# Performance work log

Measured on AMD Instinct MI355X. Metric: run time of the kernel, lower is better.

Reference implementation:

```python
import jax, jax.numpy as jnp
import numpy as np

NMOD, NVEC, R, M, B = 4, 100000, 64, 512, 16384


def setup_inputs() -> dict:
    key = jax.random.key(0)
    ks = jax.random.split(key, 9)
    indices = jax.random.randint(ks[0], (B, NMOD), 0, NVEC, dtype=jnp.int32)
    # logit(U(0,1)) init for v_hat tables
    def logit_init(k):
        u = jax.random.uniform(k, (NVEC, R), dtype=jnp.float32, minval=1e-4, maxval=1.0 - 1e-4)
        return jnp.log(u) - jnp.log1p(-u)
    v0, v1, v2, v3 = (logit_init(ks[i]) for i in range(1, 5))
    S = jax.random.normal(ks[5], (M, NMOD * R), dtype=jnp.float32) / (2 * np.pi)
    b = jax.random.uniform(ks[6], (1, M), dtype=jnp.float32, minval=0.0, maxval=2 * np.pi)
    w_mu = jax.random.uniform(ks[7], (2 * M, 1), dtype=jnp.float32)
    return {"indices": indices, "v0": v0, "v1": v1, "v2": v2, "v3": v3,
            "S": S, "b": b, "w_mu": w_mu}


def _stick_break_gather(v_hat, idx):
    # Stick-breaking weights are computed row-wise (cumsum over axis=1),
    # so gathering rows first is mathematically identical to building the
    # full table and gathering (and far cheaper).
    vh = v_hat[idx]                       # [B, R]
    log_v = jax.nn.log_sigmoid(vh)
    log_vm = jax.nn.log_sigmoid(-vh)
    excl_cumsum = jnp.cumsum(log_vm, axis=1) - log_vm  # exclusive cumsum
    return jnp.exp(log_v + excl_cumsum)   # [B, R]


def reference(indices, v0, v1, v2, v3, S, b, w_mu):
    emb = jnp.concatenate([
        _stick_break_gather(v0, indices[:, 0]),
        _stick_break_gather(v1, indices[:, 1]),
        _stick_break_gather(v2, indices[:, 2]),
        _stick_break_gather(v3, indices[:, 3]),
    ], axis=1)                             # [B, 4R]
    phi_lin = emb @ S.T + b                # [B, M]
    phi = jnp.concatenate([jnp.cos(phi_lin), jnp.sin(phi_lin)], axis=1)  # [B, 2M]
    return jax.nn.sigmoid(phi @ w_mu)      # [B, 1]
```

## Files before the change

kernel.cpp:

```cpp
#include <hip/hip_runtime.h>
#include <math.h>

#define B_TOTAL 16384
#define RR 64
#define KK 256
#define MM 512
#define ROWS 32
#define NCH 8
#define NNI 4
#define MI 2
#define ASTR 264
#define INV2PI 0.15915494309189535f

typedef __attribute__((ext_vector_type(8))) _Float16 half8;
typedef __attribute__((ext_vector_type(4))) float floatx4;

template<int CTRL, int RMASK>
static __device__ inline float dpp_mov1(float src) {
    int s = __builtin_bit_cast(int, src);
    int o = __builtin_bit_cast(int, 1.0f);
    int r = __builtin_amdgcn_update_dpp(o, s, CTRL, RMASK, 0xF, false);
    return __builtin_bit_cast(float, r);
}
template<int CTRL>
static __device__ inline float dpp_swap(float src) {
    int s = __builtin_bit_cast(int, src);
    int r = __builtin_amdgcn_update_dpp(s, s, CTRL, 0xF, 0xF, false);
    return __builtin_bit_cast(float, r);
}
static __device__ inline float red16(float x) {
    x += dpp_swap<0xB1>(x);
    x += dpp_swap<0x4E>(x);
    x += dpp_swap<0x141>(x);
    x += dpp_swap<0x140>(x);
    return x;
}

__global__ __launch_bounds__(256)
void conv_S(const float* __restrict__ S, _Float16* __restrict__ Bh)
{
    const int F = blockIdx.x * 256 + threadIdx.x;
    const int o = F >> 9;
    const int c = F & 511;
    const float* src = &S[c * KK + o * 8];
    float v[8];
    *reinterpret_cast<float4*>(&v[0]) = *reinterpret_cast<const float4*>(src);
    *reinterpret_cast<float4*>(&v[4]) = *reinterpret_cast<const float4*>(src + 4);
    half8 hv;
    #pragma unroll
    for (int j = 0; j < 8; ++j)
        hv[j] = (_Float16)(v[j] * INV2PI);
    *reinterpret_cast<half8*>(&Bh[F * 8]) = hv;
}

__global__ __launch_bounds__(512, 4)
void nest2_mfma(const int* __restrict__ indices,
                const float* __restrict__ v0, const float* __restrict__ v1,
                const float* __restrict__ v2, const float* __restrict__ v3,
                const _Float16* __restrict__ Bh,
                const float* __restrict__ bvec, const float* __restrict__ w_mu,
                float* __restrict__ out)
{
    __shared__ alignas(16) _Float16 Ah[ROWS * ASTR];
    __shared__ float red[8][ROWS];

    const int tid = threadIdx.x;
    const int rowBase = blockIdx.x * ROWS;
    const int wid  = __builtin_amdgcn_readfirstlane(tid >> 6);
    const int lane = tid & 63;
    const int l15  = lane & 15;
    const int lg   = lane >> 4;
    const int wcol0 = wid * 64;

    #define BOFF(ch, ni) ((((ch) * 4 + lg) * 512 + wcol0 + (ni) * 16 + l15) * 8)

    const int* ip = indices + rowBase * 4 + wid * 16;
    const float* vts[4] = {v0, v1, v2, v3};
    float vh[16];
    #pragma unroll
    for (int it = 0; it < 16; ++it) {
        const int mod = it & 3;
        vh[it] = vts[mod][ip[it] * RR + lane];
    }

    half8 b[NNI];
    #pragma unroll
    for (int ni = 0; ni < NNI; ++ni)
        b[ni] = *reinterpret_cast<const half8*>(&Bh[BOFF(0, ni)]);
    float bbv[NNI], wav[NNI];
    #pragma unroll
    for (int ni = 0; ni < NNI; ++ni) {
        const int c = wcol0 + ni * 16 + l15;
        const float w1 = w_mu[c];
        const float w2 = w_mu[MM + c];
        wav[ni] = sqrtf(w1 * w1 + w2 * w2);
        bbv[ni] = bvec[c] * INV2PI + atan2f(w1, w2) * INV2PI;
    }

    #pragma unroll
    for (int it = 0; it < 16; ++it) {
        const int p   = wid * 16 + it;
        const int row = p >> 2;
        const int mod = p & 3;
        const float t  = __expf(vh[it]);
        const float um = __builtin_amdgcn_rcpf(1.f + t);
        float pr = um;
        pr *= dpp_mov1<0x111, 0xF>(pr);
        pr *= dpp_mov1<0x112, 0xF>(pr);
        pr *= dpp_mov1<0x114, 0xF>(pr);
        pr *= dpp_mov1<0x118, 0xF>(pr);
        pr *= dpp_mov1<0x142, 0xA>(pr);
        pr *= dpp_mov1<0x143, 0xC>(pr);
        const float x = t * pr;
        Ah[row * ASTR + mod * RR + lane] = (_Float16)x;
    }
    __syncthreads();

    floatx4 acc[MI][NNI];
    #pragma unroll
    for (int mi = 0; mi < MI; ++mi)
        #pragma unroll
        for (int ni = 0; ni < NNI; ++ni)
            acc[mi][ni] = (floatx4){0.f, 0.f, 0.f, 0.f};

    #pragma unroll
    for (int ch = 0; ch < NCH; ++ch) {
        half8 ah[MI];
        #pragma unroll
        for (int mi = 0; mi < MI; ++mi)
            ah[mi] = *reinterpret_cast<const half8*>(
                &Ah[(mi * 16 + l15) * ASTR + ch * 32 + lg * 8]);
        half8 bn[NNI];
        if (ch + 1 < NCH) {
            #pragma unroll
            for (int ni = 0; ni < NNI; ++ni)
                bn[ni] = *reinterpret_cast<const half8*>(&Bh[BOFF(ch + 1, ni)]);
        }
        __builtin_amdgcn_s_setprio(1);
        #pragma unroll
        for (int ni = 0; ni < NNI; ++ni)
            #pragma unroll
            for (int mi = 0; mi < MI; ++mi)
                acc[mi][ni] = __builtin_amdgcn_mfma_f32_16x16x32_f16(ah[mi], b[ni], acc[mi][ni], 0, 0, 0);
        __builtin_amdgcn_s_setprio(0);
        if (ch + 1 < NCH) {
            #pragma unroll
            for (int ni = 0; ni < NNI; ++ni)
                b[ni] = bn[ni];
        }
    }

    float rp[MI][4];
    #pragma unroll
    for (int mi = 0; mi < MI; ++mi)
        #pragma unroll
        for (int r = 0; r < 4; ++r) rp[mi][r] = 0.f;

    #pragma unroll
    for (int ni = 0; ni < NNI; ++ni) {
        #pragma unroll
        for (int mi = 0; mi < MI; ++mi)
            #pragma unroll
            for (int r = 0; r < 4; ++r) {
                const float psi = acc[mi][ni][r] + bbv[ni];
                rp[mi][r] = fmaf(wav[ni], __builtin_amdgcn_sinf(psi), rp[mi][r]);
            }
    }

    #pragma unroll
    for (int mi = 0; mi < MI; ++mi)
        #pragma unroll
        for (int r = 0; r < 4; ++r) {
            const float v = red16(rp[mi][r]);
            if (l15 == 0) red[wid][mi * 16 + lg * 4 + r] = v;
        }
    __syncthreads();

    if (tid < ROWS) {
        float s = 0.f;
        #pragma unroll
        for (int w = 0; w < 8; ++w) s += red[w][tid];
        out[rowBase + tid] = 1.f / (1.f + expf(-s));
    }
    #undef BOFF
}

extern "C" void kernel_launch(void* const* d_in, const int* in_sizes, int n_in,
                              void* d_out, int out_size, void* d_ws, size_t ws_size,
                              hipStream_t stream) {
    const int*   indices = (const int*)d_in[0];
    const float* v0 = (const float*)d_in[1];
    const float* v1 = (const float*)d_in[2];
    const float* v2 = (const float*)d_in[3];
    const float* v3 = (const float*)d_in[4];
    const float* S  = (const float*)d_in[5];
    const float* bb = (const float*)d_in[6];
    const float* w  = (const float*)d_in[7];
    float* out = (float*)d_out;

    _Float16* Bh = (_Float16*)d_ws;

    hipLaunchKernelGGL(conv_S, dim3(MM * KK / (256 * 8)), dim3(256), 0, stream,
                       S, Bh);
    hipLaunchKernelGGL(nest2_mfma, dim3(B_TOTAL / ROWS), dim3(512), 0, stream,
                       indices, v0, v1, v2, v3, Bh, bb, w, out);
}
```

Before: 19.77 us.

## Split output columns across block pairs with atomic partial sums and completion flags

Each 32-row tile is now handled by two blocks that each cover half of the 512 feature columns. Partial logits are combined through atomicAdd into a workspace, and whichever block of the pair finishes second, detected with an agent-scope flag counter, applies the sigmoid. The per-column amplitude and phase (sqrt and atan2 of w_mu) are precomputed once in the prep kernel, which also zeroes the accumulators and flags. This doubles the block count and raises the occupancy hint, at the cost of duplicated gather and stick-breaking work per row, extra atomics and fences, and removal of the B-operand register prefetch.

Measured after the change: 60.04 us. 204% more time.

```diff
diff --git a/kernel.cpp b/kernel.cpp
--- a/kernel.cpp
+++ b/kernel.cpp
@@ -7,7 +7,7 @@
 #define MM 512
 #define ROWS 32
 #define NCH 8
-#define NNI 4
+#define NNI 2
 #define MI 2
 #define ASTR 264
 #define INV2PI 0.15915494309189535f
@@ -37,40 +37,65 @@
 }
 
 __global__ __launch_bounds__(256)
-void conv_S(const float* __restrict__ S, _Float16* __restrict__ Bh)
+void prep(const float* __restrict__ S, const float* __restrict__ bvec,
+          const float* __restrict__ w_mu,
+          _Float16* __restrict__ Bh, float* __restrict__ wa,
+          float* __restrict__ bb2, float* __restrict__ part,
+          int* __restrict__ flags)
 {
-    const int F = blockIdx.x * 256 + threadIdx.x;
-    const int o = F >> 9;
-    const int c = F & 511;
-    const float* src = &S[c * KK + o * 8];
-    float v[8];
-    *reinterpret_cast<float4*>(&v[0]) = *reinterpret_cast<const float4*>(src);
-    *reinterpret_cast<float4*>(&v[4]) = *reinterpret_cast<const float4*>(src + 4);
-    half8 hv;
-    #pragma unroll
-    for (int j = 0; j < 8; ++j)
-        hv[j] = (_Float16)(v[j] * INV2PI);
-    *reinterpret_cast<half8*>(&Bh[F * 8]) = hv;
-}
-
-__global__ __launch_bounds__(512, 4)
+    const int bid = blockIdx.x;
+    const int tid = threadIdx.x;
+    if (bid < 64) {
+        const int F = bid * 256 + tid;
+        const int o = F >> 9;
+        const int c = F & 511;
+        const float* src = &S[c * KK + o * 8];
+        float v[8];
+        *reinterpret_cast<float4*>(&v[0]) = *reinterpret_cast<const float4*>(src);
+        *reinterpret_cast<float4*>(&v[4]) = *reinterpret_cast<const float4*>(src + 4);
+        half8 hv;
+        #pragma unroll
+        for (int j = 0; j < 8; ++j)
+            hv[j] = (_Float16)(v[j] * INV2PI);
+        *reinterpret_cast<half8*>(&Bh[F * 8]) = hv;
+    } else if (bid == 64) {
+        #pragma unroll
+        for (int q = 0; q < 2; ++q) {
+            const int c = tid * 2 + q;
+            const float w1 = w_mu[c];
+            const float w2 = w_mu[MM + c];
+            wa[c]  = sqrtf(w1 * w1 + w2 * w2);
+            bb2[c] = bvec[c] * INV2PI + atan2f(w1, w2) * INV2PI;
+            flags[c] = 0;
+        }
+    } else {
+        float4 z = {0.f, 0.f, 0.f, 0.f};
+        *reinterpret_cast<float4*>(&part[(bid - 65) * 1024 + tid * 4]) = z;
+    }
+}
+
+__global__ __launch_bounds__(512, 8)
 void nest2_mfma(const int* __restrict__ indices,
                 const float* __restrict__ v0, const float* __restrict__ v1,
                 const float* __restrict__ v2, const float* __restrict__ v3,
                 const _Float16* __restrict__ Bh,
-                const float* __restrict__ bvec, const float* __restrict__ w_mu,
+                const float* __restrict__ wa, const float* __restrict__ bb2,
+                float* __restrict__ part, int* __restrict__ flags,
                 float* __restrict__ out)
 {
     __shared__ alignas(16) _Float16 Ah[ROWS * ASTR];
     __shared__ float red[8][ROWS];
+    __shared__ int oldflag;
 
     const int tid = threadIdx.x;
-    const int rowBase = blockIdx.x * ROWS;
+    const int pair = blockIdx.x >> 1;
+    const int half = blockIdx.x & 1;
+    const int rowBase = pair * ROWS;
     const int wid  = __builtin_amdgcn_readfirstlane(tid >> 6);
     const int lane = tid & 63;
     const int l15  = lane & 15;
     const int lg   = lane >> 4;
-    const int wcol0 = wid * 64;
+    const int wcol0 = half * 256 + wid * 32;
 
     #define BOFF(ch, ni) ((((ch) * 4 + lg) * 512 + wcol0 + (ni) * 16 + l15) * 8)
 
@@ -83,18 +108,12 @@
         vh[it] = vts[mod][ip[it] * RR + lane];
     }
 
-    half8 b[NNI];
-    #pragma unroll
-    for (int ni = 0; ni < NNI; ++ni)
-        b[ni] = *reinterpret_cast<const half8*>(&Bh[BOFF(0, ni)]);
     float bbv[NNI], wav[NNI];
     #pragma unroll
     for (int ni = 0; ni < NNI; ++ni) {
         const int c = wcol0 + ni * 16 + l15;
-        const float w1 = w_mu[c];
-        const float w2 = w_mu[MM + c];
-        wav[ni] = sqrtf(w1 * w1 + w2 * w2);
-        bbv[ni] = bvec[c] * INV2PI + atan2f(w1, w2) * INV2PI;
+        wav[ni] = wa[c];
+        bbv[ni] = bb2[c];
     }
 
     #pragma unroll
@@ -130,12 +149,10 @@
         for (int mi = 0; mi < MI; ++mi)
             ah[mi] = *reinterpret_cast<const half8*>(
                 &Ah[(mi * 16 + l15) * ASTR + ch * 32 + lg * 8]);
-        half8 bn[NNI];
-        if (ch + 1 < NCH) {
-            #pragma unroll
-            for (int ni = 0; ni < NNI; ++ni)
-                bn[ni] = *reinterpret_cast<const half8*>(&Bh[BOFF(ch + 1, ni)]);
-        }
+        half8 b[NNI];
+        #pragma unroll
+        for (int ni = 0; ni < NNI; ++ni)
+            b[ni] = *reinterpret_cast<const half8*>(&Bh[BOFF(ch, ni)]);
         __builtin_amdgcn_s_setprio(1);
         #pragma unroll
         for (int ni = 0; ni < NNI; ++ni)
@@ -143,11 +160,6 @@
             for (int mi = 0; mi < MI; ++mi)
                 acc[mi][ni] = __builtin_amdgcn_mfma_f32_16x16x32_f16(ah[mi], b[ni], acc[mi][ni], 0, 0, 0);
         __builtin_amdgcn_s_setprio(0);
-        if (ch + 1 < NCH) {
-            #pragma unroll
-            for (int ni = 0; ni < NNI; ++ni)
-                b[ni] = bn[ni];
-        }
     }
 
     float rp[MI][4];
@@ -180,7 +192,22 @@
         float s = 0.f;
         #pragma unroll
         for (int w = 0; w < 8; ++w) s += red[w][tid];
-        out[rowBase + tid] = 1.f / (1.f + expf(-s));
+        atomicAdd(&part[rowBase + tid], s);
+    }
+    __syncthreads();
+    if (tid == 0) {
+        __threadfence();
+        oldflag = __hip_atomic_fetch_add(&flags[pair], 1,
+                                         __ATOMIC_ACQ_REL,
+                                         __HIP_MEMORY_SCOPE_AGENT);
+    }
+    __syncthreads();
+    if (oldflag == 1 && tid < ROWS) {
+        __threadfence();
+        const float s = __hip_atomic_load(&part[rowBase + tid],
+                                          __ATOMIC_RELAXED,
+                                          __HIP_MEMORY_SCOPE_AGENT);
+        out[rowBase + tid] = 1.f / (1.f + __expf(-s));
     }
     #undef BOFF
 }
@@ -198,10 +225,15 @@
     const float* w  = (const float*)d_in[7];
     float* out = (float*)d_out;
 
-    _Float16* Bh = (_Float16*)d_ws;
-
-    hipLaunchKernelGGL(conv_S, dim3(MM * KK / (256 * 8)), dim3(256), 0, stream,
-                       S, Bh);
-    hipLaunchKernelGGL(nest2_mfma, dim3(B_TOTAL / ROWS), dim3(512), 0, stream,
-                       indices, v0, v1, v2, v3, Bh, bb, w, out);
-}
+    char* wsb = (char*)d_ws;
+    _Float16* Bh  = (_Float16*)wsb;
+    float*    wa  = (float*)(wsb + 262144);
+    float*    bb2 = (float*)(wsb + 264192);
+    float*    part= (float*)(wsb + 266240);
+    int*      flg = (int*)(wsb + 331776);
+
+    hipLaunchKernelGGL(prep, dim3(81), dim3(256), 0, stream,
+                       S, bb, w, Bh, wa, bb2, part, flg);
+    hipLaunchKernelGGL(nest2_mfma, dim3(B_TOTAL / ROWS * 2), dim3(512), 0, stream,
+                       indices, v0, v1, v2, v3, Bh, wa, bb2, part, flg, out);
+}
```

## Fuse S conversion into main kernel with grid-wide atomic barrier

Applied to the files above, without the earlier changes.

Removes the separate conv_S launch. Each of the 512 blocks now converts a slice of S to fp16 and precomputes one column's amplitude and phase (sqrt and atan2 of w_mu) into workspace. All blocks then wait on a global atomic counter before the MFMA phase, and the counter is reset by a memset before launch. This saves a kernel launch and the redundant per-thread atan2 work, but it adds a memset, a spin-wait grid barrier, and a deadlock risk if the 512 blocks of 512 threads cannot all be co-resident.

Result: slower. 50.31 us (median of 2 runs) (+154.4%).

```diff
diff --git a/kernel.cpp b/kernel.cpp
--- a/kernel.cpp
+++ b/kernel.cpp
@@ -6,6 +6,7 @@
 #define KK 256
 #define MM 512
 #define ROWS 32
+#define NBLK (B_TOTAL / ROWS)
 #define NCH 8
 #define NNI 4
 #define MI 2
@@ -36,36 +37,22 @@
     return x;
 }
 
-__global__ __launch_bounds__(256)
-void conv_S(const float* __restrict__ S, _Float16* __restrict__ Bh)
-{
-    const int F = blockIdx.x * 256 + threadIdx.x;
-    const int o = F >> 9;
-    const int c = F & 511;
-    const float* src = &S[c * KK + o * 8];
-    float v[8];
-    *reinterpret_cast<float4*>(&v[0]) = *reinterpret_cast<const float4*>(src);
-    *reinterpret_cast<float4*>(&v[4]) = *reinterpret_cast<const float4*>(src + 4);
-    half8 hv;
-    #pragma unroll
-    for (int j = 0; j < 8; ++j)
-        hv[j] = (_Float16)(v[j] * INV2PI);
-    *reinterpret_cast<half8*>(&Bh[F * 8]) = hv;
-}
-
 __global__ __launch_bounds__(512, 4)
-void nest2_mfma(const int* __restrict__ indices,
-                const float* __restrict__ v0, const float* __restrict__ v1,
-                const float* __restrict__ v2, const float* __restrict__ v3,
-                const _Float16* __restrict__ Bh,
-                const float* __restrict__ bvec, const float* __restrict__ w_mu,
-                float* __restrict__ out)
+void nest2_fused(const int* __restrict__ indices,
+                 const float* __restrict__ v0, const float* __restrict__ v1,
+                 const float* __restrict__ v2, const float* __restrict__ v3,
+                 const float* __restrict__ S,
+                 const float* __restrict__ bvec, const float* __restrict__ w_mu,
+                 _Float16* __restrict__ Bh, float* __restrict__ wa,
+                 float* __restrict__ bb2, int* __restrict__ done,
+                 float* __restrict__ out)
 {
     __shared__ alignas(16) _Float16 Ah[ROWS * ASTR];
     __shared__ float red[8][ROWS];
 
     const int tid = threadIdx.x;
-    const int rowBase = blockIdx.x * ROWS;
+    const int bid = blockIdx.x;
+    const int rowBase = bid * ROWS;
     const int wid  = __builtin_amdgcn_readfirstlane(tid >> 6);
     const int lane = tid & 63;
     const int l15  = lane & 15;
@@ -74,6 +61,26 @@
 
     #define BOFF(ch, ni) ((((ch) * 4 + lg) * 512 + wcol0 + (ni) * 16 + l15) * 8)
 
+    if (tid < 32) {
+        const int F = bid * 32 + tid;
+        const int o = F >> 9;
+        const int c = F & 511;
+        const float* src = &S[c * KK + o * 8];
+        float v[8];
+        *reinterpret_cast<float4*>(&v[0]) = *reinterpret_cast<const float4*>(src);
+        *reinterpret_cast<float4*>(&v[4]) = *reinterpret_cast<const float4*>(src + 4);
+        half8 hv;
+        #pragma unroll
+        for (int j = 0; j < 8; ++j)
+            hv[j] = (_Float16)(v[j] * INV2PI);
+        *reinterpret_cast<half8*>(&Bh[F * 8]) = hv;
+    } else if (tid == 32) {
+        const float w1 = w_mu[bid];
+        const float w2 = w_mu[MM + bid];
+        wa[bid]  = sqrtf(w1 * w1 + w2 * w2);
+        bb2[bid] = bvec[bid] * INV2PI + atan2f(w1, w2) * INV2PI;
+    }
+
     const int* ip = indices + rowBase * 4 + wid * 16;
     const float* vts[4] = {v0, v1, v2, v3};
     float vh[16];
@@ -81,20 +88,6 @@
     for (int it = 0; it < 16; ++it) {
         const int mod = it & 3;
         vh[it] = vts[mod][ip[it] * RR + lane];
-    }
-
-    half8 b[NNI];
-    #pragma unroll
-    for (int ni = 0; ni < NNI; ++ni)
-        b[ni] = *reinterpret_cast<const half8*>(&Bh[BOFF(0, ni)]);
-    float bbv[NNI], wav[NNI];
-    #pragma unroll
-    for (int ni = 0; ni < NNI; ++ni) {
-        const int c = wcol0 + ni * 16 + l15;
-        const float w1 = w_mu[c];
-        const float w2 = w_mu[MM + c];
-        wav[ni] = sqrtf(w1 * w1 + w2 * w2);
-        bbv[ni] = bvec[c] * INV2PI + atan2f(w1, w2) * INV2PI;
     }
 
     #pragma unroll
@@ -116,12 +109,36 @@
     }
     __syncthreads();
 
+    if (tid == 0) {
+        __threadfence();
+        __hip_atomic_fetch_add(done, 1, __ATOMIC_RELEASE,
+                               __HIP_MEMORY_SCOPE_AGENT);
+        while (__hip_atomic_load(done, __ATOMIC_RELAXED,
+                                 __HIP_MEMORY_SCOPE_AGENT) < NBLK)
+            __builtin_amdgcn_s_sleep(32);
+        __threadfence();
+    }
+    __syncthreads();
+
+    float bbv[NNI], wav[NNI];
+    #pragma unroll
+    for (int ni = 0; ni < NNI; ++ni) {
+        const int c = wcol0 + ni * 16 + l15;
+        wav[ni] = wa[c];
+        bbv[ni] = bb2[c];
+    }
+
     floatx4 acc[MI][NNI];
     #pragma unroll
     for (int mi = 0; mi < MI; ++mi)
         #pragma unroll
         for (int ni = 0; ni < NNI; ++ni)
             acc[mi][ni] = (floatx4){0.f, 0.f, 0.f, 0.f};
+
+    half8 b[NNI];
+    #pragma unroll
+    for (int ni = 0; ni < NNI; ++ni)
+        b[ni] = *reinterpret_cast<const half8*>(&Bh[BOFF(0, ni)]);
 
     #pragma unroll
     for (int ch = 0; ch < NCH; ++ch) {
@@ -180,7 +197,7 @@
         float s = 0.f;
         #pragma unroll
         for (int w = 0; w < 8; ++w) s += red[w][tid];
-        out[rowBase + tid] = 1.f / (1.f + expf(-s));
+        out[rowBase + tid] = 1.f / (1.f + __expf(-s));
     }
     #undef BOFF
 }
@@ -198,10 +215,14 @@
     const float* w  = (const float*)d_in[7];
     float* out = (float*)d_out;
 
-    _Float16* Bh = (_Float16*)d_ws;
-
-    hipLaunchKernelGGL(conv_S, dim3(MM * KK / (256 * 8)), dim3(256), 0, stream,
-                       S, Bh);
-    hipLaunchKernelGGL(nest2_mfma, dim3(B_TOTAL / ROWS), dim3(512), 0, stream,
-                       indices, v0, v1, v2, v3, Bh, bb, w, out);
-}
+    char* wsb = (char*)d_ws;
+    _Float16* Bh  = (_Float16*)wsb;
+    float*    wa  = (float*)(wsb + 262144);
+    float*    bb2 = (float*)(wsb + 264192);
+    int*      done= (int*)(wsb + 266240);
+
+    hipMemsetAsync(done, 0, sizeof(int), stream);
+    hipLaunchKernelGGL(nest2_fused, dim3(NBLK), dim3(512), 0, stream,
+                       indices, v0, v1, v2, v3, S, bb, w,
+                       Bh, wa, bb2, done, out);
+}
```
